# Kernel optimization log

Measured on AMD Instinct MI355X. Metric: run time of the kernel, lower is better.

## Reference

```python
import jax, jax.numpy as jnp
import numpy as np

DM = 1024        # model dim
E = 32           # totalexperts = expertsets*nexperts = 8*4
FE = 128         # expertsize
T = 4            # sparsity = nexperts (tokens per group)
EPS_TIEBREAK = 1e-6


def setup_inputs() -> dict:
    key = jax.random.key(0)
    k0, k1, k2, k3 = jax.random.split(key, 4)
    x = jax.random.normal(k0, (4, 4096, DM), dtype=jnp.float32)
    # fan_in-style inits matching misc.get_init_weight / get_init_bias
    controller = jax.random.normal(k1, (DM, E), dtype=jnp.float32) / np.float32(np.sqrt(DM))
    f1 = jax.random.normal(k2, (DM, E, FE), dtype=jnp.float32) / np.float32(np.sqrt(DM))
    bias = jnp.zeros((E, FE), dtype=jnp.float32)
    f2 = jax.random.normal(k3, (E, FE, DM), dtype=jnp.float32) / np.float32(np.sqrt(E * FE / T))
    return {"x": x, "controller": controller, "f1": f1, "bias": bias, "f2": f2}


def reference(x, controller, f1, bias, f2):
    B, S, d = x.shape
    t = T
    g = S // t
    # '... (b t) d -> ... b t d'
    grouped = x.reshape(B, g, t, d)
    # controller logits: '... t d, d e -> ... t e'
    logits = jnp.einsum('bgtd,de->bgte', grouped, controller)
    # deterministic tie-break offset over the t (slot) axis
    logits = logits + jnp.linspace(0.0, EPS_TIEBREAK, t, dtype=logits.dtype)[:, None]
    # softmax over dim=1 (group axis) as in original
    probs = jax.nn.softmax(logits, axis=1)
    # hard argmax mask over dim=-3 (group axis), scaled by soft probs
    perm = (logits == jnp.max(logits, axis=1, keepdims=True)).astype(x.dtype) * probs
    # expert up-projection with soft permutation: '... t d, d e f, ... t e -> ... e f'
    inner = jnp.einsum('bgtd,def,bgte->bgef', grouped, f1, perm)
    inner = jax.nn.relu(inner + bias)
    # expert down-projection: '... e f, e f d -> ... e d'
    inter = jnp.einsum('bgef,efd->bged', inner, f2)
    # unpermute: '... e d, ... t e -> ... t d'
    res = jnp.einsum('bged,bgte->bgtd', inter, perm)
    return res.reshape(B, S, d)
```

## Files before the change

### kernel.cpp

```cpp
#include <hip/hip_runtime.h>
#include <math.h>


#define DM   1024
#define NE   32
#define FE   128
#define T4   4
#define SS   4096
#define NGRP 1024
#define NROW 512
#define LP_STRIDE (NROW * NGRP)
#define VP_OFF   524288

__global__ __launch_bounds__(256, 2)
void k_logits(const float* __restrict__ x, const float* __restrict__ ctrl,
              float* __restrict__ Lp, float* __restrict__ out)
{
    const int m      = blockIdx.x;
    const int ks     = blockIdx.y;
    const int tid    = threadIdx.x;
    const int base_s = m * 128;
    const int b      = base_s >> 12;
    const int g0     = (base_s & 4095) >> 2;

    __shared__ float xT[64 * 132];
    __shared__ float cs[64 * 32];

    const int tokg = tid & 31;
    const int eg   = tid >> 5;

    float acc[4][4];
#pragma unroll
    for (int i = 0; i < 4; ++i)
#pragma unroll
        for (int j = 0; j < 4; ++j) acc[i][j] = 0.f;

    const int row0 = tid >> 2;
    const int f4i  = tid & 3;

    for (int kit = 0; kit < 4; ++kit) {
        const int k0 = ks * 256 + kit * 64;
        __syncthreads();
#pragma unroll
        for (int rr = 0; rr < 2; ++rr) {
            const int row = row0 + rr * 64;
            const float* xp = x + (size_t)(base_s + row) * DM + k0;
#pragma unroll
            for (int cr = 0; cr < 4; ++cr) {
                const int col = f4i + cr * 4;
                const float4 v = *(const float4*)(xp + col * 4);
                const int d = col * 4;
                xT[(d + 0) * 132 + row] = v.x;
                xT[(d + 1) * 132 + row] = v.y;
                xT[(d + 2) * 132 + row] = v.z;
                xT[(d + 3) * 132 + row] = v.w;
            }
        }
        {
            const float4* cg = (const float4*)(ctrl + (size_t)k0 * NE);
            float4* cl = (float4*)cs;
            cl[tid]       = cg[tid];
            cl[tid + 256] = cg[tid + 256];
        }
        __syncthreads();
#pragma unroll 8
        for (int d = 0; d < 64; ++d) {
            const float4 xv = *(const float4*)(xT + d * 132 + tokg * 4);
            const float4 cv = *(const float4*)(cs + d * 32 + eg * 4);
            const float xa[4] = { xv.x, xv.y, xv.z, xv.w };
            const float ca[4] = { cv.x, cv.y, cv.z, cv.w };
#pragma unroll
            for (int i = 0; i < 4; ++i)
#pragma unroll
                for (int j = 0; j < 4; ++j) acc[i][j] += xa[i] * ca[j];
        }
    }

    {
        float* Lb = Lp + (size_t)ks * LP_STRIDE;
        const int g = g0 + tokg;
#pragma unroll
        for (int i = 0; i < 4; ++i)
#pragma unroll
            for (int j = 0; j < 4; ++j) {
                const int row = (b * T4 + i) * NE + eg * 4 + j;
                Lb[(size_t)row * NGRP + g] = acc[i][j];
            }
    }

    {
        const float4 z = make_float4(0.f, 0.f, 0.f, 0.f);
        float4* o4 = (float4*)(out + (size_t)(base_s + ks * 32) * DM);
#pragma unroll 4
        for (int i = tid; i < 32 * DM / 4; i += 256) o4[i] = z;
    }
}

__global__ __launch_bounds__(128)
void k_route(float* __restrict__ Lp)
{
    const int r    = blockIdx.x * 2 + (threadIdx.x >> 6);
    const int lane = threadIdx.x & 63;
    const float* L0 = Lp + (size_t)r * NGRP;

    float mx = -INFINITY, s = 0.f;
    int gm = 0;
#pragma unroll
    for (int c = 0; c < 4; ++c) {
        const int g0c = c * 256 + lane * 4;
        const float4 v0 = *(const float4*)(L0 + g0c);
        const float4 v1 = *(const float4*)(L0 + 1 * LP_STRIDE + g0c);
        const float4 v2 = *(const float4*)(L0 + 2 * LP_STRIDE + g0c);
        const float4 v3 = *(const float4*)(L0 + 3 * LP_STRIDE + g0c);
        const float l[4] = { v0.x + v1.x + v2.x + v3.x,
                             v0.y + v1.y + v2.y + v3.y,
                             v0.z + v1.z + v2.z + v3.z,
                             v0.w + v1.w + v2.w + v3.w };
#pragma unroll
        for (int j = 0; j < 4; ++j) {
            const float lv = l[j];
            if (lv > mx) { s = s * __expf(mx - lv) + 1.f; mx = lv; gm = g0c + j; }
            else         { s += __expf(lv - mx); }
        }
    }
#pragma unroll
    for (int off = 1; off < 64; off <<= 1) {
        const float m2 = __shfl_xor(mx, off);
        const float s2 = __shfl_xor(s, off);
        const int   g2 = __shfl_xor(gm, off);
        const float mn = fmaxf(mx, m2);
        s  = s * __expf(mx - mn) + s2 * __expf(m2 - mn);
        gm = (m2 > mx) ? g2 : ((m2 == mx && g2 < gm) ? g2 : gm);
        mx = mn;
    }
    if (lane == 0) {
        ((int*)Lp)[(size_t)r * NGRP] = gm;
        Lp[(size_t)r * NGRP + 1] = 1.f / s;
    }
}

__global__ __launch_bounds__(256, 2)
void k_up(const float* __restrict__ x, const float* __restrict__ f1,
          float* __restrict__ ws)
{
    const int e   = blockIdx.x & 31;
    const int dc  = blockIdx.x >> 5;
    const int tid = threadIdx.x;

    __shared__ float xs[16 * 68];
    __shared__ int   gS[16];

    if (tid < 16) {
        const int b = tid >> 2, t = tid & 3;
        const int r = (b * T4 + t) * NE + e;
        gS[tid] = ((const int*)ws)[(size_t)r * NGRP];
    }
    __syncthreads();

    {
        const int row = tid >> 4;
        const int f4c = tid & 15;
        const int b = row >> 2, t = row & 3;
        const int s = b * SS + gS[row] * 4 + t;
        const float4 v = *(const float4*)(x + (size_t)s * DM + dc * 64 + f4c * 4);
        xs[row * 68 + f4c * 4 + 0] = v.x;
        xs[row * 68 + f4c * 4 + 1] = v.y;
        xs[row * 68 + f4c * 4 + 2] = v.z;
        xs[row * 68 + f4c * 4 + 3] = v.w;
    }
    __syncthreads();

    const int f4 = tid & 31;
    const int rw = tid >> 5;
    const float* f1p = f1 + (size_t)(dc * 64) * (NE * FE) + e * FE + f4 * 4;
    const float* x0 = xs + (rw * 2) * 68;
    const float* x1 = xs + (rw * 2 + 1) * 68;

    float a0[4] = {0.f, 0.f, 0.f, 0.f}, a1[4] = {0.f, 0.f, 0.f, 0.f};
#pragma unroll 8
    for (int dl = 0; dl < 64; ++dl) {
        const float4 w4 = *(const float4*)(f1p + (size_t)dl * (NE * FE));
        const float xa = x0[dl], xb = x1[dl];
        a0[0] += xa * w4.x; a0[1] += xa * w4.y; a0[2] += xa * w4.z; a0[3] += xa * w4.w;
        a1[0] += xb * w4.x; a1[1] += xb * w4.y; a1[2] += xb * w4.z; a1[3] += xb * w4.w;
    }

    float* Vp = ws + VP_OFF + (size_t)(dc * 32 + e) * (16 * FE);
    *(float4*)(Vp + (rw * 2)     * FE + f4 * 4) = make_float4(a0[0], a0[1], a0[2], a0[3]);
    *(float4*)(Vp + (rw * 2 + 1) * FE + f4 * 4) = make_float4(a1[0], a1[1], a1[2], a1[3]);
}

__global__ __launch_bounds__(256, 2)
void k_down(const float* __restrict__ f2, const float* __restrict__ bias,
            const float* __restrict__ ws, float* __restrict__ out)
{
    const int e   = blockIdx.x & 31;
    const int dt  = blockIdx.x >> 5;
    const int tid = threadIdx.x;

    __shared__ float vv[16 * 132];
    __shared__ float hh[16 * 132];
    __shared__ int   gS[16];
    __shared__ float pS[16];

    if (tid < 16) {
        const int b = tid >> 2, t = tid & 3;
        const int r = (b * T4 + t) * NE + e;
        gS[tid] = ((const int*)ws)[(size_t)r * NGRP];
        pS[tid] = ws[(size_t)r * NGRP + 1];
    }

    {
        const float* Vp = ws + VP_OFF;
#pragma unroll
        for (int q = 0; q < 8; ++q) {
            const int i = tid + q * 256;
            float s = 0.f;
#pragma unroll
            for (int dc = 0; dc < 16; ++dc)
                s += Vp[(size_t)(dc * 32 + e) * (16 * FE) + i];
            vv[(i >> 7) * 132 + (i & 127)] = s;
        }
    }
    __syncthreads();

    if (tid < 128) {
        const int f = tid;
        const float bv = bias[e * FE + f];
#pragma unroll
        for (int b = 0; b < 4; ++b) {
            int   g[T4]; float p[T4], vl[T4];
#pragma unroll
            for (int t = 0; t < T4; ++t) {
                g[t] = gS[b * 4 + t]; p[t] = pS[b * 4 + t];
                vl[t] = vv[(b * 4 + t) * 132 + f];
            }
#pragma unroll
            for (int t = 0; t < T4; ++t) {
                float u = bv;
#pragma unroll
                for (int t2 = 0; t2 < T4; ++t2)
                    if (g[t2] == g[t]) u += p[t2] * vl[t2];
                hh[(b * 4 + t) * 132 + f] = fmaxf(u, 0.f);
            }
        }
    }
    __syncthreads();

    const int d4 = tid & 31;
    const int rw = tid >> 5;
    const float* f2p = f2 + (size_t)e * FE * DM + dt * 128 + d4 * 4;
    const float* h0 = hh + (rw * 2) * 132;
    const float* h1 = hh + (rw * 2 + 1) * 132;

    float a0[4] = {0.f, 0.f, 0.f, 0.f}, a1[4] = {0.f, 0.f, 0.f, 0.f};
#pragma unroll 8
    for (int f = 0; f < FE; ++f) {
        const float4 w4 = *(const float4*)(f2p + (size_t)f * DM);
        const float ha = h0[f], hb = h1[f];
        a0[0] += ha * w4.x; a0[1] += ha * w4.y; a0[2] += ha * w4.z; a0[3] += ha * w4.w;
        a1[0] += hb * w4.x; a1[1] += hb * w4.y; a1[2] += hb * w4.z; a1[3] += hb * w4.w;
    }

#pragma unroll
    for (int h = 0; h < 2; ++h) {
        const int row = rw * 2 + h;
        const int b = row >> 2, t = row & 3;
        const float p = pS[row];
        const float* a = h ? a1 : a0;
        float* orow = out + ((size_t)(b * SS + gS[row] * 4 + t)) * DM + dt * 128 + d4 * 4;
        atomicAdd(orow + 0, p * a[0]);
        atomicAdd(orow + 1, p * a[1]);
        atomicAdd(orow + 2, p * a[2]);
        atomicAdd(orow + 3, p * a[3]);
    }
}

extern "C" void kernel_launch(void* const* d_in, const int* in_sizes, int n_in,
                              void* d_out, int out_size, void* d_ws, size_t ws_size,
                              hipStream_t stream)
{
    const float* x    = (const float*)d_in[0];
    const float* ctrl = (const float*)d_in[1];
    const float* f1   = (const float*)d_in[2];
    const float* bias = (const float*)d_in[3];
    const float* f2   = (const float*)d_in[4];
    float* out = (float*)d_out;
    float* ws  = (float*)d_ws;

    k_logits<<<dim3(128, 4), 256, 0, stream>>>(x, ctrl, ws, out);
    k_route <<<dim3(256),    128, 0, stream>>>(ws);
    k_up    <<<dim3(512),    256, 0, stream>>>(x, f1, ws);
    k_down  <<<dim3(256),    256, 0, stream>>>(f2, bias, ws, out);
}
```

Measured before the change: 199.9 us.

## Split kernels into smaller blocks and factor activation into its own kernel

Halves the per-block work in the logits, up-projection and down-projection kernels so the grids grow (e.g. 512→1024, 256→512 blocks), giving more parallelism across the GPU's compute units. The bias/ReLU/permutation step moves out of k_down into a new k_act kernel that writes pre-scaled hidden activations to workspace, so k_down no longer redundantly reduces the up-projection partials per d-tile. This costs an extra kernel launch and a workspace round trip, and each block now reuses f1/f2 weight loads across fewer rows.

```diff
diff --git a/kernel.cpp b/kernel.cpp
--- a/kernel.cpp
+++ b/kernel.cpp
@@ -11,29 +11,28 @@
 #define NROW 512
 #define LP_STRIDE (NROW * NGRP)
 #define VP_OFF   524288
-
-__global__ __launch_bounds__(256, 2)
+#define HH_OFF   1572864
+
+__global__ __launch_bounds__(256, 4)
 void k_logits(const float* __restrict__ x, const float* __restrict__ ctrl,
               float* __restrict__ Lp, float* __restrict__ out)
 {
     const int m      = blockIdx.x;
     const int ks     = blockIdx.y;
     const int tid    = threadIdx.x;
-    const int base_s = m * 128;
+    const int base_s = m * 64;
     const int b      = base_s >> 12;
     const int g0     = (base_s & 4095) >> 2;
 
-    __shared__ float xT[64 * 132];
+    __shared__ float xT[64 * 68];
     __shared__ float cs[64 * 32];
 
-    const int tokg = tid & 31;
-    const int eg   = tid >> 5;
-
-    float acc[4][4];
-#pragma unroll
-    for (int i = 0; i < 4; ++i)
-#pragma unroll
-        for (int j = 0; j < 4; ++j) acc[i][j] = 0.f;
+    const int tq = tid & 15;
+    const int eg = tid >> 4;
+
+    float acc[4][2];
+#pragma unroll
+    for (int i = 0; i < 4; ++i) { acc[i][0] = 0.f; acc[i][1] = 0.f; }
 
     const int row0 = tid >> 2;
     const int f4i  = tid & 3;
@@ -41,19 +40,17 @@
     for (int kit = 0; kit < 4; ++kit) {
         const int k0 = ks * 256 + kit * 64;
         __syncthreads();
-#pragma unroll
-        for (int rr = 0; rr < 2; ++rr) {
-            const int row = row0 + rr * 64;
-            const float* xp = x + (size_t)(base_s + row) * DM + k0;
+        {
+            const float* xp = x + (size_t)(base_s + row0) * DM + k0;
 #pragma unroll
             for (int cr = 0; cr < 4; ++cr) {
                 const int col = f4i + cr * 4;
                 const float4 v = *(const float4*)(xp + col * 4);
                 const int d = col * 4;
-                xT[(d + 0) * 132 + row] = v.x;
-                xT[(d + 1) * 132 + row] = v.y;
-                xT[(d + 2) * 132 + row] = v.z;
-                xT[(d + 3) * 132 + row] = v.w;
+                xT[(d + 0) * 68 + row0] = v.x;
+                xT[(d + 1) * 68 + row0] = v.y;
+                xT[(d + 2) * 68 + row0] = v.z;
+                xT[(d + 3) * 68 + row0] = v.w;
             }
         }
         {
@@ -65,34 +62,34 @@
         __syncthreads();
 #pragma unroll 8
         for (int d = 0; d < 64; ++d) {
-            const float4 xv = *(const float4*)(xT + d * 132 + tokg * 4);
-            const float4 cv = *(const float4*)(cs + d * 32 + eg * 4);
+            const float4 xv = *(const float4*)(xT + d * 68 + tq * 4);
+            const float2 cv = *(const float2*)(cs + d * 32 + eg * 2);
             const float xa[4] = { xv.x, xv.y, xv.z, xv.w };
-            const float ca[4] = { cv.x, cv.y, cv.z, cv.w };
-#pragma unroll
-            for (int i = 0; i < 4; ++i)
-#pragma unroll
-                for (int j = 0; j < 4; ++j) acc[i][j] += xa[i] * ca[j];
+#pragma unroll
+            for (int i = 0; i < 4; ++i) {
+                acc[i][0] += xa[i] * cv.x;
+                acc[i][1] += xa[i] * cv.y;
+            }
         }
     }
 
     {
         float* Lb = Lp + (size_t)ks * LP_STRIDE;
-        const int g = g0 + tokg;
+        const int g = g0 + tq;
 #pragma unroll
         for (int i = 0; i < 4; ++i)
 #pragma unroll
-            for (int j = 0; j < 4; ++j) {
-                const int row = (b * T4 + i) * NE + eg * 4 + j;
+            for (int j = 0; j < 2; ++j) {
+                const int row = (b * T4 + i) * NE + eg * 2 + j;
                 Lb[(size_t)row * NGRP + g] = acc[i][j];
             }
     }
 
     {
         const float4 z = make_float4(0.f, 0.f, 0.f, 0.f);
-        float4* o4 = (float4*)(out + (size_t)(base_s + ks * 32) * DM);
+        float4* o4 = (float4*)(out + (size_t)(base_s + ks * 16) * DM);
 #pragma unroll 4
-        for (int i = tid; i < 32 * DM / 4; i += 256) o4[i] = z;
+        for (int i = tid; i < 16 * DM / 4; i += 256) o4[i] = z;
     }
 }
 
@@ -139,29 +136,30 @@
     }
 }
 
-__global__ __launch_bounds__(256, 2)
+__global__ __launch_bounds__(256, 4)
 void k_up(const float* __restrict__ x, const float* __restrict__ f1,
           float* __restrict__ ws)
 {
     const int e   = blockIdx.x & 31;
-    const int dc  = blockIdx.x >> 5;
+    const int dc  = (blockIdx.x >> 5) & 15;
+    const int rh  = blockIdx.x >> 9;
     const int tid = threadIdx.x;
 
-    __shared__ float xs[16 * 68];
-    __shared__ int   gS[16];
-
-    if (tid < 16) {
-        const int b = tid >> 2, t = tid & 3;
-        const int r = (b * T4 + t) * NE + e;
+    __shared__ float xs[8 * 68];
+    __shared__ int   gS[8];
+
+    if (tid < 8) {
+        const int r = (rh * 8 + tid) * NE + e;
         gS[tid] = ((const int*)ws)[(size_t)r * NGRP];
     }
     __syncthreads();
 
-    {
+    if (tid < 128) {
         const int row = tid >> 4;
         const int f4c = tid & 15;
-        const int b = row >> 2, t = row & 3;
-        const int s = b * SS + gS[row] * 4 + t;
+        const int grow = rh * 8 + row;
+        const int bq = grow >> 2, t = grow & 3;
+        const int s = bq * SS + gS[row] * 4 + t;
         const float4 v = *(const float4*)(x + (size_t)s * DM + dc * 64 + f4c * 4);
         xs[row * 68 + f4c * 4 + 0] = v.x;
         xs[row * 68 + f4c * 4 + 1] = v.y;
@@ -173,107 +171,107 @@
     const int f4 = tid & 31;
     const int rw = tid >> 5;
     const float* f1p = f1 + (size_t)(dc * 64) * (NE * FE) + e * FE + f4 * 4;
-    const float* x0 = xs + (rw * 2) * 68;
-    const float* x1 = xs + (rw * 2 + 1) * 68;
-
-    float a0[4] = {0.f, 0.f, 0.f, 0.f}, a1[4] = {0.f, 0.f, 0.f, 0.f};
-#pragma unroll 8
+    const float* xp  = xs + rw * 68;
+
+    float a[4] = {0.f, 0.f, 0.f, 0.f};
+#pragma unroll 16
     for (int dl = 0; dl < 64; ++dl) {
         const float4 w4 = *(const float4*)(f1p + (size_t)dl * (NE * FE));
-        const float xa = x0[dl], xb = x1[dl];
-        a0[0] += xa * w4.x; a0[1] += xa * w4.y; a0[2] += xa * w4.z; a0[3] += xa * w4.w;
-        a1[0] += xb * w4.x; a1[1] += xb * w4.y; a1[2] += xb * w4.z; a1[3] += xb * w4.w;
+        const float xa = xp[dl];
+        a[0] += xa * w4.x; a[1] += xa * w4.y; a[2] += xa * w4.z; a[3] += xa * w4.w;
     }
 
     float* Vp = ws + VP_OFF + (size_t)(dc * 32 + e) * (16 * FE);
-    *(float4*)(Vp + (rw * 2)     * FE + f4 * 4) = make_float4(a0[0], a0[1], a0[2], a0[3]);
-    *(float4*)(Vp + (rw * 2 + 1) * FE + f4 * 4) = make_float4(a1[0], a1[1], a1[2], a1[3]);
-}
-
-__global__ __launch_bounds__(256, 2)
-void k_down(const float* __restrict__ f2, const float* __restrict__ bias,
-            const float* __restrict__ ws, float* __restrict__ out)
+    *(float4*)(Vp + (rh * 8 + rw) * FE + f4 * 4) = make_float4(a[0], a[1], a[2], a[3]);
+}
+
+__global__ __launch_bounds__(256, 4)
+void k_act(const float* __restrict__ bias, float* __restrict__ ws)
 {
     const int e   = blockIdx.x & 31;
-    const int dt  = blockIdx.x >> 5;
+    const int b   = blockIdx.x >> 5;
     const int tid = threadIdx.x;
 
-    __shared__ float vv[16 * 132];
-    __shared__ float hh[16 * 132];
-    __shared__ int   gS[16];
-    __shared__ float pS[16];
-
-    if (tid < 16) {
-        const int b = tid >> 2, t = tid & 3;
-        const int r = (b * T4 + t) * NE + e;
+    __shared__ float vv[T4][FE];
+    __shared__ int   gS[T4];
+    __shared__ float pS[T4];
+
+    if (tid < 4) {
+        const int r = (b * T4 + tid) * NE + e;
         gS[tid] = ((const int*)ws)[(size_t)r * NGRP];
         pS[tid] = ws[(size_t)r * NGRP + 1];
     }
 
+    const float* Vp = ws + VP_OFF;
+#pragma unroll
+    for (int q = 0; q < 2; ++q) {
+        const int idx = tid + q * 256;
+        const int t = idx >> 7, f = idx & 127;
+        float s = 0.f;
+#pragma unroll
+        for (int dc = 0; dc < 16; ++dc)
+            s += Vp[(size_t)(dc * 32 + e) * (16 * FE) + (b * T4 + t) * FE + f];
+        vv[t][f] = s;
+    }
+    __syncthreads();
+
+#pragma unroll
+    for (int q = 0; q < 2; ++q) {
+        const int idx = tid + q * 256;
+        const int t = idx >> 7, f = idx & 127;
+        float u = bias[e * FE + f];
+#pragma unroll
+        for (int t2 = 0; t2 < T4; ++t2)
+            if (gS[t2] == gS[t]) u += pS[t2] * vv[t2][f];
+        ws[HH_OFF + (size_t)e * (16 * FE) + (b * T4 + t) * FE + f] =
+            pS[t] * fmaxf(u, 0.f);
+    }
+}
+
+__global__ __launch_bounds__(256, 2)
+void k_down(const float* __restrict__ f2, const float* __restrict__ ws,
+            float* __restrict__ out)
+{
+    const int e   = blockIdx.x & 31;
+    const int dt  = (blockIdx.x >> 5) & 7;
+    const int rh  = blockIdx.x >> 8;
+    const int tid = threadIdx.x;
+
+    __shared__ float hs[8 * FE];
+    __shared__ int   gS[8];
+
+    if (tid < 8) {
+        const int r = (rh * 8 + tid) * NE + e;
+        gS[tid] = ((const int*)ws)[(size_t)r * NGRP];
+    }
     {
-        const float* Vp = ws + VP_OFF;
-#pragma unroll
-        for (int q = 0; q < 8; ++q) {
-            const int i = tid + q * 256;
-            float s = 0.f;
-#pragma unroll
-            for (int dc = 0; dc < 16; ++dc)
-                s += Vp[(size_t)(dc * 32 + e) * (16 * FE) + i];
-            vv[(i >> 7) * 132 + (i & 127)] = s;
-        }
-    }
-    __syncthreads();
-
-    if (tid < 128) {
-        const int f = tid;
-        const float bv = bias[e * FE + f];
-#pragma unroll
-        for (int b = 0; b < 4; ++b) {
-            int   g[T4]; float p[T4], vl[T4];
-#pragma unroll
-            for (int t = 0; t < T4; ++t) {
-                g[t] = gS[b * 4 + t]; p[t] = pS[b * 4 + t];
-                vl[t] = vv[(b * 4 + t) * 132 + f];
-            }
-#pragma unroll
-            for (int t = 0; t < T4; ++t) {
-                float u = bv;
-#pragma unroll
-                for (int t2 = 0; t2 < T4; ++t2)
-                    if (g[t2] == g[t]) u += p[t2] * vl[t2];
-                hh[(b * 4 + t) * 132 + f] = fmaxf(u, 0.f);
-            }
-        }
+        const int row = tid >> 5, f4 = tid & 31;
+        const float4 v = *(const float4*)(ws + HH_OFF + (size_t)e * (16 * FE)
+                                             + (rh * 8 + row) * FE + f4 * 4);
+        *(float4*)(hs + row * FE + f4 * 4) = v;
     }
     __syncthreads();
 
     const int d4 = tid & 31;
     const int rw = tid >> 5;
     const float* f2p = f2 + (size_t)e * FE * DM + dt * 128 + d4 * 4;
-    const float* h0 = hh + (rw * 2) * 132;
-    const float* h1 = hh + (rw * 2 + 1) * 132;
-
-    float a0[4] = {0.f, 0.f, 0.f, 0.f}, a1[4] = {0.f, 0.f, 0.f, 0.f};
-#pragma unroll 8
+    const float* hp  = hs + rw * FE;
+
+    float a[4] = {0.f, 0.f, 0.f, 0.f};
+#pragma unroll 16
     for (int f = 0; f < FE; ++f) {
         const float4 w4 = *(const float4*)(f2p + (size_t)f * DM);
-        const float ha = h0[f], hb = h1[f];
-        a0[0] += ha * w4.x; a0[1] += ha * w4.y; a0[2] += ha * w4.z; a0[3] += ha * w4.w;
-        a1[0] += hb * w4.x; a1[1] += hb * w4.y; a1[2] += hb * w4.z; a1[3] += hb * w4.w;
-    }
-
-#pragma unroll
-    for (int h = 0; h < 2; ++h) {
-        const int row = rw * 2 + h;
-        const int b = row >> 2, t = row & 3;
-        const float p = pS[row];
-        const float* a = h ? a1 : a0;
-        float* orow = out + ((size_t)(b * SS + gS[row] * 4 + t)) * DM + dt * 128 + d4 * 4;
-        atomicAdd(orow + 0, p * a[0]);
-        atomicAdd(orow + 1, p * a[1]);
-        atomicAdd(orow + 2, p * a[2]);
-        atomicAdd(orow + 3, p * a[3]);
-    }
+        const float ha = hp[f];
+        a[0] += ha * w4.x; a[1] += ha * w4.y; a[2] += ha * w4.z; a[3] += ha * w4.w;
+    }
+
+    const int grow = rh * 8 + rw;
+    const int bq = grow >> 2, t = grow & 3;
+    float* orow = out + ((size_t)(bq * SS + gS[rw] * 4 + t)) * DM + dt * 128 + d4 * 4;
+    atomicAdd(orow + 0, a[0]);
+    atomicAdd(orow + 1, a[1]);
+    atomicAdd(orow + 2, a[2]);
+    atomicAdd(orow + 3, a[3]);
 }
 
 extern "C" void kernel_launch(void* const* d_in, const int* in_sizes, int n_in,
@@ -288,8 +286,9 @@
     float* out = (float*)d_out;
     float* ws  = (float*)d_ws;
 
-    k_logits<<<dim3(128, 4), 256, 0, stream>>>(x, ctrl, ws, out);
+    k_logits<<<dim3(256, 4), 256, 0, stream>>>(x, ctrl, ws, out);
     k_route <<<dim3(256),    128, 0, stream>>>(ws);
-    k_up    <<<dim3(512),    256, 0, stream>>>(x, f1, ws);
-    k_down  <<<dim3(256),    256, 0, stream>>>(f2, bias, ws, out);
-}
+    k_up    <<<dim3(1024),   256, 0, stream>>>(x, f1, ws);
+    k_act   <<<dim3(128),    256, 0, stream>>>(bias, ws);
+    k_down  <<<dim3(512),    256, 0, stream>>>(f2, ws, out);
+}
```

Measured after the change: 193.1 us. 1.03x faster.
